# Kernel tuning notes

Measured on AMD Instinct MI355X. Metric: run time of the kernel, lower is better.

Reference implementation:

```python
import jax, jax.numpy as jnp
import numpy as np
from jax import lax

B, N, C, H, W, D, BEV = 2, 6, 64, 128, 352, 48, 64


def _make_buffers():
    # depths: linspace(1,100,D) -> used with shape (1,1,D,1)
    depths = jnp.linspace(1.0, 100.0, D).reshape(1, 1, D, 1)
    y, x = jnp.meshgrid(jnp.arange(H), jnp.arange(W), indexing='ij')
    xy1 = jnp.stack((x.flatten(), y.flatten(), jnp.ones(H * W)), axis=0).astype(jnp.float32)  # (3, H*W)
    return depths, xy1


def setup_inputs() -> dict:
    key = jax.random.key(0)
    ks = jax.random.split(key, 8)
    image_features = jax.random.normal(ks[0], (B * N, C, H, W), jnp.float32)
    # realistic invertible pinhole intrinsics embedded in 4x4
    fx = 500.0 + 10.0 * jax.random.normal(ks[1], (B, N))
    fy = 500.0 + 10.0 * jax.random.normal(ks[2], (B, N))
    K = jnp.tile(jnp.eye(4, dtype=jnp.float32), (B, N, 1, 1))
    K = K.at[..., 0, 0].set(fx).at[..., 1, 1].set(fy)
    K = K.at[..., 0, 2].set(W / 2.0).at[..., 1, 2].set(H / 2.0)
    extrinsics = jnp.tile(jnp.eye(4, dtype=jnp.float32), (B, N, 1, 1)) + 0.01 * jax.random.normal(ks[3], (B, N, 4, 4))
    view_attention = jnp.ones((1, N, 1, H, W), jnp.float32)
    depth_attention = jnp.ones((1, D, 1, 1), jnp.float32)
    # kaiming-normal conv weights (fan_in mode, relu gain sqrt(2))
    c1w = jax.random.normal(ks[4], (BEV, 3, 3, 3), jnp.float32) * np.sqrt(2.0 / (3 * 9))
    c1b = jnp.zeros((BEV,), jnp.float32)
    c2w = jax.random.normal(ks[5], (BEV, BEV, 3, 3), jnp.float32) * np.sqrt(2.0 / (BEV * 9))
    c2b = jnp.zeros((BEV,), jnp.float32)
    bn1_g = jnp.ones((BEV,), jnp.float32); bn1_b = jnp.zeros((BEV,), jnp.float32)
    bn2_g = jnp.ones((BEV,), jnp.float32); bn2_b = jnp.zeros((BEV,), jnp.float32)
    depths, xy1 = _make_buffers()
    return dict(image_features=image_features, intrinsics=K, extrinsics=extrinsics,
                view_attention=view_attention, depth_attention=depth_attention,
                c1w=c1w, c1b=c1b, bn1_g=bn1_g, bn1_b=bn1_b,
                c2w=c2w, c2b=c2b, bn2_g=bn2_g, bn2_b=bn2_b,
                depths=depths, xy1=xy1)


def _conv3x3(x, w, b):
    y = lax.conv_general_dilated(x, w, (1, 1), 'SAME',
                                 dimension_numbers=('NCHW', 'OIHW', 'NCHW'))
    return y + b.reshape(1, -1, 1, 1)


def _bn_train(x, g, b, eps=1e-5):
    # torch BatchNorm2d in training mode: biased batch stats over (B,H,W)
    m = x.mean(axis=(0, 2, 3), keepdims=True)
    v = x.var(axis=(0, 2, 3), keepdims=True)
    return g.reshape(1, -1, 1, 1) * (x - m) * lax.rsqrt(v + eps) + b.reshape(1, -1, 1, 1)


def reference(image_features, intrinsics, extrinsics, view_attention, depth_attention,
              c1w, c1b, bn1_g, bn1_b, c2w, c2b, bn2_g, bn2_b, depths, xy1):
    BN = B * N
    # ---- lift ----
    K3 = intrinsics.reshape(BN, 4, 4)[:, :3, :3]
    Kinv = jnp.linalg.inv(K3)                          # (BN,3,3)
    rays = jnp.einsum('bij,jp->bip', Kinv, xy1)        # (BN,3,H*W)
    # depths (1,1,D,1) * rays (BN,3,1,HW) -> (BN,3,D,HW), then the original's
    # .view(B,N,3,H,W,D) (a raw row-major reshape, reproduced faithfully)
    pc = (depths * rays[:, :, None, :]).reshape(B, N, 3, H, W, D)
    # (depth_probs in the original is computed then discarded; omitted)
    # ---- splat (fused weighted reduction over N and D) ----
    da = jax.nn.softmax(depth_attention, axis=1).reshape(D)       # (D,)
    va = jax.nn.softmax(view_attention, axis=1)[0, :, 0]          # (N,H,W)
    bev_features = jnp.einsum('bnchwd,d,nhw->bchw', pc, da, va)   # (B,3,H,W)
    h = jax.nn.relu(_bn_train(_conv3x3(bev_features, c1w, c1b), bn1_g, bn1_b))
    bev = jax.nn.relu(_bn_train(_conv3x3(h, c2w, c2b), bn2_g, bn2_b))
    return pc, bev
```

## Files before the change

kernel.cpp:

```cpp
#include <hip/hip_runtime.h>

#define W_ 352
#define H_ 128
#define HW 45056
#define D_ 48
#define B_ 2
#define N_ 6
#define DHW (D_*HW)
#define PC_SIZE (36*DHW)
#define BHW (B_*HW)
#define BEVN (B_*64*HW)

#define WS_KINV 0
#define WS_SUM1 192
#define WS_SQ1  256
#define WS_SUM2 448
#define WS_SQ2  512

#define NPC_BLK (PC_SIZE/1024)
#define CH_H2B0 4096
#define CH_H2B1 (CH_H2B0 + BEVN/2048)

typedef unsigned short ushort_t;
typedef __attribute__((ext_vector_type(8))) short bf16x8;
typedef __attribute__((ext_vector_type(4))) float f32x4;
typedef __attribute__((ext_vector_type(8))) unsigned short u16x8;
typedef __attribute__((ext_vector_type(4))) unsigned short u16x4;

static __device__ inline ushort_t f2bf(float f) {
    union { float f; unsigned u; } v; v.f = f;
    unsigned r = v.u + 0x7FFF + ((v.u >> 16) & 1);
    return (ushort_t)(r >> 16);
}
static __device__ inline float bf2f(ushort_t u) {
    union { unsigned u; float f; } v; v.u = ((unsigned)u) << 16; return v.f;
}
static __device__ inline void invert3x3(const float* __restrict__ M, float* __restrict__ o) {
    float a = M[0], b = M[1], c = M[2];
    float d = M[4], e = M[5], f = M[6];
    float g = M[8], h = M[9], ii = M[10];
    float det = a*(e*ii - f*h) - b*(d*ii - f*g) + c*(d*h - e*g);
    float inv = 1.f / det;
    o[0] = (e*ii - f*h)*inv; o[1] = (c*h - b*ii)*inv; o[2] = (b*f - c*e)*inv;
    o[3] = (f*g - d*ii)*inv; o[4] = (a*ii - c*g)*inv; o[5] = (c*d - a*f)*inv;
    o[6] = (d*h - e*g)*inv;  o[7] = (b*g - a*h)*inv;  o[8] = (a*e - b*d)*inv;
}

static __device__ inline void pc_write(int pcblk, const float* __restrict__ ws,
                                       const float* __restrict__ depths,
                                       float* __restrict__ out) {
    int f = pcblk * 1024 + (int)threadIdx.x * 4;
    int bnc = f / DHW;
    int r1  = f - bnc * DHW;
    int d   = r1 / HW;
    int p   = r1 - d * HW;
    int y   = p / W_;
    int x   = p - y * W_;
    float ka = ws[WS_KINV + bnc * 3 + 0];
    float kb = ws[WS_KINV + bnc * 3 + 1];
    float kc = ws[WS_KINV + bnc * 3 + 2];
    float dep = depths[d];
    float base = fmaf(kb, (float)y, kc);
    f32x4 v;
    v.x = dep * fmaf(ka, (float)(x + 0), base);
    v.y = dep * fmaf(ka, (float)(x + 1), base);
    v.z = dep * fmaf(ka, (float)(x + 2), base);
    v.w = dep * fmaf(ka, (float)(x + 3), base);
    __builtin_nontemporal_store(v, (f32x4*)(out + f));
}

__global__ __launch_bounds__(256) void k_fused1(const float* __restrict__ K4,
                                                const float* __restrict__ datt,
                                                const float* __restrict__ vatt,
                                                const float* __restrict__ depths,
                                                const float* __restrict__ w1,
                                                const float* __restrict__ b1,
                                                const float* __restrict__ w2,
                                                float* __restrict__ ws,
                                                ushort_t* __restrict__ h1pm,
                                                ushort_t* __restrict__ packedW) {
    int bid = blockIdx.x, tid = threadIdx.x;
    if (bid >= 352) {
        int e = (bid - 352) * 256 + tid;
        int tap = e >> 12;
        int r   = e & 4095;
        int n   = r >> 6, k = r & 63;
        int slot = (k >> 3) ^ (n & 7);
        packedW[tap * 4096 + n * 64 + slot * 8 + (k & 7)] = f2bf(w2[(n * 64 + k) * 9 + tap]);
        return;
    }
    if (bid == 0 && tid >= 128 && tid < 140)
        invert3x3(K4 + (tid - 128) * 16, ws + WS_KINV + (tid - 128) * 9);

    __shared__ float sBev[3][10][34];
    __shared__ float wl[64 * 27];
    __shared__ float sDep[48], sDa[48], sKinv[54];
    __shared__ __align__(16) ushort_t sTile[256 * 64];
    __shared__ float sSum[64], sSq[64];

    int b  = bid / 176;
    int t0 = bid - b * 176;
    int ty = t0 / 11, tx = t0 - ty * 11;
    int y0 = ty * 8, x0 = tx * 32;

    if (tid < 48) sDep[tid] = depths[tid];
    if (tid < 64) { sSum[tid] = 0.f; sSq[tid] = 0.f; }
    if (tid >= 64 && tid < 70) invert3x3(K4 + (b * 6 + tid - 64) * 16, sKinv + (tid - 64) * 9);
    if (tid == 192) {
        float mx = -1e30f;
        for (int k = 0; k < D_; k++) mx = fmaxf(mx, datt[k]);
        float s = 0.f, e[D_];
        for (int k = 0; k < D_; k++) { e[k] = expf(datt[k] - mx); s += e[k]; }
        float invs = 1.f / s;
        for (int k = 0; k < D_; k++) sDa[k] = e[k] * invs;
    }
    for (int i = tid; i < 64 * 27; i += 256) wl[i] = w1[i];
    __syncthreads();

    for (int idx = tid; idx < 340; idx += 256) {
        int hy = idx / 34, hx = idx - hy * 34;
        int py = y0 + hy - 1, px = x0 + hx - 1;
        float a0 = 0.f, a1 = 0.f, a2 = 0.f;
        if ((unsigned)py < H_ && (unsigned)px < W_) {
            int pix = py * W_ + px;
            float va[N_]; float mx = -1e30f;
            for (int n = 0; n < N_; n++) { va[n] = vatt[n * HW + pix]; mx = fmaxf(mx, va[n]); }
            float s = 0.f;
            for (int n = 0; n < N_; n++) { va[n] = expf(va[n] - mx); s += va[n]; }
            float invs = 1.f / s;
            int q0 = pix * 48;
            int d = q0 / HW;
            int p = q0 - d * HW;
            int y = p / W_;
            int x = p - y * W_;
            float fx = (float)x, fy = (float)y;
            float S0 = 0.f, S1 = 0.f, S2 = 0.f;
            #pragma unroll
            for (int dd = 0; dd < D_; dd++) {
                float wq = sDa[dd] * sDep[d];
                S0 = fmaf(wq, fx, S0);
                S1 = fmaf(wq, fy, S1);
                S2 += wq;
                x++; fx += 1.f;
                if (x == W_) { x = 0; fx = 0.f; y++; fy += 1.f; if (y == H_) { y = 0; fy = 0.f; d++; } }
            }
            for (int n = 0; n < N_; n++) {
                float van = va[n] * invs;
                const float* kv = sKinv + n * 9;
                a0 = fmaf(van, fmaf(kv[0], S0, fmaf(kv[1], S1, kv[2] * S2)), a0);
                a1 = fmaf(van, fmaf(kv[3], S0, fmaf(kv[4], S1, kv[5] * S2)), a1);
                a2 = fmaf(van, fmaf(kv[6], S0, fmaf(kv[7], S1, kv[8] * S2)), a2);
            }
        }
        sBev[0][hy][hx] = a0;
        sBev[1][hy][hx] = a1;
        sBev[2][hy][hx] = a2;
    }
    __syncthreads();

    int oy = tid >> 5, ox = tid & 31;
    int y = y0 + oy, x = x0 + ox;
    float v[27];
    #pragma unroll
    for (int ci = 0; ci < 3; ci++)
        #pragma unroll
        for (int dy = 0; dy < 3; dy++)
            #pragma unroll
            for (int dx = 0; dx < 3; dx++)
                v[ci * 9 + dy * 3 + dx] = sBev[ci][oy + dy][ox + dx];
    u16x8 pack[8];
    #pragma unroll
    for (int co = 0; co < 64; co++) {
        float acc = b1[co];
        #pragma unroll
        for (int k = 0; k < 27; k++) acc = fmaf(wl[co * 27 + k], v[k], acc);
        pack[co >> 3][co & 7] = (short)f2bf(acc);
    }
    ushort_t* dst = h1pm + (size_t)(b * HW + y * W_ + x) * 64;
    #pragma unroll
    for (int j = 0; j < 8; j++) {
        *(u16x8*)(dst + j * 8) = pack[j];
        *(u16x8*)(&sTile[tid * 64 + j * 8]) = pack[j];
    }
    __syncthreads();

    int c8 = tid & 7;
    int lp = tid >> 3;
    float s[8] = {0,0,0,0,0,0,0,0}, q[8] = {0,0,0,0,0,0,0,0};
    for (int p = lp; p < 256; p += 32) {
        u16x8 vv = *(const u16x8*)(&sTile[p * 64 + c8 * 8]);
        #pragma unroll
        for (int e = 0; e < 8; e++) {
            float f = bf2f(vv[e]);
            s[e] += f;
            q[e] = fmaf(f, f, q[e]);
        }
    }
    #pragma unroll
    for (int e = 0; e < 8; e++) {
        s[e] += __shfl_xor(s[e], 8);  s[e] += __shfl_xor(s[e], 16); s[e] += __shfl_xor(s[e], 32);
        q[e] += __shfl_xor(q[e], 8);  q[e] += __shfl_xor(q[e], 16); q[e] += __shfl_xor(q[e], 32);
    }
    if ((tid & 56) == 0) {
        #pragma unroll
        for (int e = 0; e < 8; e++) {
            atomicAdd(&sSum[c8 * 8 + e], s[e]);
            atomicAdd(&sSq[c8 * 8 + e], q[e]);
        }
    }
    __syncthreads();
    if (tid < 64) {
        atomicAdd(ws + WS_SUM1 + tid, sSum[tid]);
        atomicAdd(ws + WS_SQ1 + tid, sSq[tid]);
    }
}

__global__ __launch_bounds__(256) void k_conv2(const ushort_t* __restrict__ h1pm,
                                               const ushort_t* __restrict__ packedW,
                                               const float* __restrict__ b2,
                                               const float* __restrict__ g1,
                                               const float* __restrict__ bb1,
                                               float* __restrict__ ws,
                                               ushort_t* __restrict__ h2b) {
    __shared__ __align__(16) ushort_t sA[204 * 64];
    __shared__ __align__(16) ushort_t sB[3 * 4096];
    __shared__ float sSc[64], sSh[64];
    __shared__ float sRs[4][64], sRq[4][64];

    const int tid = threadIdx.x;
    if (tid < 64) {
        const float invM = 1.f / (float)BHW;
        float m = ws[WS_SUM1 + tid] * invM;
        float var = ws[WS_SQ1 + tid] * invM - m * m;
        float sc = g1[tid] * rsqrtf(var + 1e-5f);
        sSc[tid] = sc;
        sSh[tid] = bb1[tid] - m * sc;
    }
    __syncthreads();

    const int bid = blockIdx.x;
    const int b  = bid / 352;
    const int r0 = bid - b * 352;
    const int yb = r0 / 11;
    const int xb = r0 - yb * 11;
    const int x0 = xb * 32;
    const int y0 = yb * 4;
    const ushort_t* h1p = h1pm + (size_t)b * HW * 64;

    for (int idx = tid; idx < 204 * 8; idx += 256) {
        int r  = idx >> 3;
        int c8 = idx & 7;
        int hy = r / 34;
        int hx = r - hy * 34;
        int py = y0 + hy - 1, px = x0 + hx - 1;
        u16x8 ov = {0, 0, 0, 0, 0, 0, 0, 0};
        if ((unsigned)py < H_ && (unsigned)px < W_) {
            u16x8 v = *(const u16x8*)(h1p + (size_t)(py * W_ + px) * 64 + c8 * 8);
            #pragma unroll
            for (int e = 0; e < 8; e++) {
                int ci = c8 * 8 + e;
                float f = fmaxf(fmaf(sSc[ci], bf2f(v[e]), sSh[ci]), 0.f);
                ov[e] = (short)f2bf(f);
            }
        }
        int slot = c8 ^ (r & 7);
        *(u16x8*)(&sA[r * 64 + slot * 8]) = ov;
    }

    const int w    = tid >> 6;
    const int lane = tid & 63;
    const int g    = lane >> 4;
    const int c16  = lane & 15;

    f32x4 acc[2][4];
    #pragma unroll
    for (int m = 0; m < 2; m++)
        #pragma unroll
        for (int n = 0; n < 4; n++)
            acc[m][n] = (f32x4){0.f, 0.f, 0.f, 0.f};

    for (int grp = 0; grp < 3; grp++) {
        __syncthreads();
        const uint4* src = (const uint4*)(packedW + grp * 3 * 4096);
        uint4* dst = (uint4*)sB;
        #pragma unroll
        for (int i = 0; i < 6; i++) dst[tid + 256 * i] = src[tid + 256 * i];
        __syncthreads();
        #pragma unroll
        for (int tt = 0; tt < 3; tt++) {
            bf16x8 afr[2][2];
            #pragma unroll
            for (int mrep = 0; mrep < 2; mrep++)
                #pragma unroll
                for (int kk = 0; kk < 2; kk++) {
                    int r = (w + grp) * 34 + tt + c16 + 16 * mrep;
                    int slot = (g + 4 * kk) ^ (r & 7);
                    afr[mrep][kk] = *(const bf16x8*)(&sA[r * 64 + slot * 8]);
                }
            #pragma unroll
            for (int nrep = 0; nrep < 4; nrep++) {
                int n = 16 * nrep + c16;
                #pragma unroll
                for (int kk = 0; kk < 2; kk++) {
                    int slot = (g + 4 * kk) ^ (n & 7);
                    bf16x8 bfr = *(const bf16x8*)(&sB[tt * 4096 + n * 64 + slot * 8]);
                    #pragma unroll
                    for (int mrep = 0; mrep < 2; mrep++)
                        acc[mrep][nrep] = __builtin_amdgcn_mfma_f32_16x16x32_bf16(
                            afr[mrep][kk], bfr, acc[mrep][nrep], 0, 0, 0);
                }
            }
        }
    }

    const int y = y0 + w;
    #pragma unroll
    for (int nrep = 0; nrep < 4; nrep++) {
        int co = 16 * nrep + c16;
        float bias = b2[co];
        ushort_t* dstrow = h2b + (size_t)(b * 64 + co) * HW + y * W_;
        float s = 0.f, q = 0.f;
        #pragma unroll
        for (int mrep = 0; mrep < 2; mrep++) {
            u16x4 ov;
            #pragma unroll
            for (int j = 0; j < 4; j++) {
                float val = acc[mrep][nrep][j] + bias;
                s += val;
                q = fmaf(val, val, q);
                ov[j] = f2bf(val);
            }
            *(u16x4*)(dstrow + x0 + 16 * mrep + g * 4) = ov;
        }
        s += __shfl_xor(s, 16); s += __shfl_xor(s, 32);
        q += __shfl_xor(q, 16); q += __shfl_xor(q, 32);
        if (g == 0) { sRs[w][co] = s; sRq[w][co] = q; }
    }
    __syncthreads();
    if (tid < 64) {
        float s = sRs[0][tid] + sRs[1][tid] + sRs[2][tid] + sRs[3][tid];
        float q = sRq[0][tid] + sRq[1][tid] + sRq[2][tid] + sRq[3][tid];
        atomicAdd(ws + WS_SUM2 + tid, s);
        atomicAdd(ws + WS_SQ2 + tid, q);
    }
}

__global__ __launch_bounds__(256) void k_tail(const float* __restrict__ depths,
                                              const float* __restrict__ ws,
                                              const float* __restrict__ g2,
                                              const float* __restrict__ bb2,
                                              float* __restrict__ out) {
    int bid = blockIdx.x, tid = threadIdx.x;
    if (bid >= CH_H2B0 && bid < CH_H2B1) {
        const ushort_t* h2b = (const ushort_t*)((const char*)out + ((size_t)CH_H2B0 * 4096));
        int f2 = (bid - CH_H2B0) * 2048 + tid * 8;
        int c = (f2 / HW) & 63;
        const float invM = 1.f / (float)BHW;
        float m = ws[WS_SUM2 + c] * invM;
        float var = ws[WS_SQ2 + c] * invM - m * m;
        float sc = g2[c] * rsqrtf(var + 1e-5f);
        float sh = bb2[c] - m * sc;
        u16x8 v = *(const u16x8*)(h2b + f2);
        float* bev = out + PC_SIZE;
        f32x4 a, d;
        a.x = fmaxf(fmaf(sc, bf2f(v[0]), sh), 0.f);
        a.y = fmaxf(fmaf(sc, bf2f(v[1]), sh), 0.f);
        a.z = fmaxf(fmaf(sc, bf2f(v[2]), sh), 0.f);
        a.w = fmaxf(fmaf(sc, bf2f(v[3]), sh), 0.f);
        d.x = fmaxf(fmaf(sc, bf2f(v[4]), sh), 0.f);
        d.y = fmaxf(fmaf(sc, bf2f(v[5]), sh), 0.f);
        d.z = fmaxf(fmaf(sc, bf2f(v[6]), sh), 0.f);
        d.w = fmaxf(fmaf(sc, bf2f(v[7]), sh), 0.f);
        *(f32x4*)(bev + f2) = a;
        *(f32x4*)(bev + f2 + 4) = d;
        __syncthreads();
        pc_write(bid, ws, depths, out);
        return;
    }
    pc_write(bid, ws, depths, out);
}

extern "C" void kernel_launch(void* const* d_in, const int* in_sizes, int n_in,
                              void* d_out, int out_size, void* d_ws, size_t ws_size,
                              hipStream_t stream) {
    const float* K4     = (const float*)d_in[1];
    const float* vatt   = (const float*)d_in[3];
    const float* datt   = (const float*)d_in[4];
    const float* c1w    = (const float*)d_in[5];
    const float* c1b    = (const float*)d_in[6];
    const float* g1     = (const float*)d_in[7];
    const float* bb1    = (const float*)d_in[8];
    const float* c2w    = (const float*)d_in[9];
    const float* c2b    = (const float*)d_in[10];
    const float* g2     = (const float*)d_in[11];
    const float* bb2    = (const float*)d_in[12];
    const float* depths = (const float*)d_in[13];

    float* ws  = (float*)d_ws;
    char* base = (char*)d_out;
    ushort_t* h1pm    = (ushort_t*)base;
    ushort_t* packedW = (ushort_t*)(base + (12u << 20));
    ushort_t* h2b     = (ushort_t*)(base + ((size_t)CH_H2B0 * 4096));

    hipMemsetAsync(ws, 0, 640 * sizeof(float), stream);
    k_fused1<<<496, 256, 0, stream>>>(K4, datt, vatt, depths, c1w, c1b, c2w, ws, h1pm, packedW);
    k_conv2 <<<704, 256, 0, stream>>>(h1pm, packedW, c2b, g1, bb1, ws, h2b);
    k_tail  <<<NPC_BLK, 256, 0, stream>>>(depths, ws, g2, bb2, (float*)d_out);
}
```

Before: 123.2 us.

## Closed-form depth sums, per-block BN partials, larger conv2 tiles, drop memset

```diff
diff --git a/kernel.cpp b/kernel.cpp
--- a/kernel.cpp
+++ b/kernel.cpp
@@ -12,14 +12,11 @@
 #define BEVN (B_*64*HW)
 
 #define WS_KINV 0
-#define WS_SUM1 192
-#define WS_SQ1  256
 #define WS_SUM2 448
 #define WS_SQ2  512
 
 #define NPC_BLK (PC_SIZE/1024)
 #define CH_H2B0 4096
-#define CH_H2B1 (CH_H2B0 + BEVN/2048)
 
 typedef unsigned short ushort_t;
 typedef __attribute__((ext_vector_type(8))) short bf16x8;
@@ -78,9 +75,11 @@
                                                 const float* __restrict__ w2,
                                                 float* __restrict__ ws,
                                                 ushort_t* __restrict__ h1pm,
-                                                ushort_t* __restrict__ packedW) {
+                                                ushort_t* __restrict__ packedW,
+                                                float* __restrict__ P1) {
     int bid = blockIdx.x, tid = threadIdx.x;
     if (bid >= 352) {
+        if (bid == 352 && tid < 128) ws[WS_SUM2 + tid] = 0.f;
         int e = (bid - 352) * 256 + tid;
         int tap = e >> 12;
         int r   = e & 4095;
@@ -95,6 +94,7 @@
     __shared__ float sBev[3][10][34];
     __shared__ float wl[64 * 27];
     __shared__ float sDep[48], sDa[48], sKinv[54];
+    __shared__ float sSumDa, sKsum;
     __shared__ __align__(16) ushort_t sTile[256 * 64];
     __shared__ float sSum[64], sSq[64];
 
@@ -112,7 +112,14 @@
         float s = 0.f, e[D_];
         for (int k = 0; k < D_; k++) { e[k] = expf(datt[k] - mx); s += e[k]; }
         float invs = 1.f / s;
-        for (int k = 0; k < D_; k++) sDa[k] = e[k] * invs;
+        float sum = 0.f, ks = 0.f;
+        for (int k = 0; k < D_; k++) {
+            float dv = e[k] * invs;
+            sDa[k] = dv;
+            sum += dv;
+            ks = fmaf(dv, (float)k, ks);
+        }
+        sSumDa = sum; sKsum = ks;
     }
     for (int i = tid; i < 64 * 27; i += 256) wl[i] = w1[i];
     __syncthreads();
@@ -133,16 +140,24 @@
             int p = q0 - d * HW;
             int y = p / W_;
             int x = p - y * W_;
-            float fx = (float)x, fy = (float)y;
-            float S0 = 0.f, S1 = 0.f, S2 = 0.f;
-            #pragma unroll
-            for (int dd = 0; dd < D_; dd++) {
-                float wq = sDa[dd] * sDep[d];
-                S0 = fmaf(wq, fx, S0);
-                S1 = fmaf(wq, fy, S1);
-                S2 += wq;
-                x++; fx += 1.f;
-                if (x == W_) { x = 0; fx = 0.f; y++; fy += 1.f; if (y == H_) { y = 0; fy = 0.f; d++; } }
+            float S0, S1, S2;
+            if (x <= W_ - 48) {
+                float dep = sDep[d];
+                S2 = dep * sSumDa;
+                S0 = dep * fmaf(sSumDa, (float)x, sKsum);
+                S1 = (float)y * S2;
+            } else {
+                float fx = (float)x, fy = (float)y;
+                S0 = 0.f; S1 = 0.f; S2 = 0.f;
+                #pragma unroll
+                for (int dd = 0; dd < D_; dd++) {
+                    float wq = sDa[dd] * sDep[d];
+                    S0 = fmaf(wq, fx, S0);
+                    S1 = fmaf(wq, fy, S1);
+                    S2 += wq;
+                    x++; fx += 1.f;
+                    if (x == W_) { x = 0; fx = 0.f; y++; fy += 1.f; if (y == H_) { y = 0; fy = 0.f; d++; } }
+                }
             }
             for (int n = 0; n < N_; n++) {
                 float van = va[n] * invs;
@@ -210,8 +225,8 @@
     }
     __syncthreads();
     if (tid < 64) {
-        atomicAdd(ws + WS_SUM1 + tid, sSum[tid]);
-        atomicAdd(ws + WS_SQ1 + tid, sSq[tid]);
+        P1[bid * 128 + tid]      = sSum[tid];
+        P1[bid * 128 + 64 + tid] = sSq[tid];
     }
 }
 
@@ -220,34 +235,48 @@
                                                const float* __restrict__ b2,
                                                const float* __restrict__ g1,
                                                const float* __restrict__ bb1,
+                                               const float* __restrict__ P1,
                                                float* __restrict__ ws,
                                                ushort_t* __restrict__ h2b) {
-    __shared__ __align__(16) ushort_t sA[204 * 64];
+    __shared__ __align__(16) ushort_t sA[340 * 64];
     __shared__ __align__(16) ushort_t sB[3 * 4096];
     __shared__ float sSc[64], sSh[64];
+    __shared__ float sPS[4][64], sPQ[4][64];
     __shared__ float sRs[4][64], sRq[4][64];
 
     const int tid = threadIdx.x;
+    {
+        int c = tid & 63, hf = tid >> 6;
+        float s = 0.f, q = 0.f;
+        #pragma unroll 4
+        for (int i = 0; i < 88; i++) {
+            const float* pp = P1 + (size_t)(hf * 88 + i) * 128;
+            s += pp[c];
+            q += pp[64 + c];
+        }
+        sPS[hf][c] = s; sPQ[hf][c] = q;
+    }
+    __syncthreads();
     if (tid < 64) {
         const float invM = 1.f / (float)BHW;
-        float m = ws[WS_SUM1 + tid] * invM;
-        float var = ws[WS_SQ1 + tid] * invM - m * m;
-        float sc = g1[tid] * rsqrtf(var + 1e-5f);
+        float m = (sPS[0][tid] + sPS[1][tid] + sPS[2][tid] + sPS[3][tid]) * invM;
+        float vv = (sPQ[0][tid] + sPQ[1][tid] + sPQ[2][tid] + sPQ[3][tid]) * invM - m * m;
+        float sc = g1[tid] * rsqrtf(vv + 1e-5f);
         sSc[tid] = sc;
         sSh[tid] = bb1[tid] - m * sc;
     }
     __syncthreads();
 
     const int bid = blockIdx.x;
-    const int b  = bid / 352;
-    const int r0 = bid - b * 352;
+    const int b  = bid / 176;
+    const int r0 = bid - b * 176;
     const int yb = r0 / 11;
     const int xb = r0 - yb * 11;
     const int x0 = xb * 32;
-    const int y0 = yb * 4;
+    const int y0 = yb * 8;
     const ushort_t* h1p = h1pm + (size_t)b * HW * 64;
 
-    for (int idx = tid; idx < 204 * 8; idx += 256) {
+    for (int idx = tid; idx < 340 * 8; idx += 256) {
         int r  = idx >> 3;
         int c8 = idx & 7;
         int hy = r / 34;
@@ -272,12 +301,14 @@
     const int g    = lane >> 4;
     const int c16  = lane & 15;
 
-    f32x4 acc[2][4];
-    #pragma unroll
-    for (int m = 0; m < 2; m++)
-        #pragma unroll
-        for (int n = 0; n < 4; n++)
-            acc[m][n] = (f32x4){0.f, 0.f, 0.f, 0.f};
+    f32x4 acc[2][2][4];
+    #pragma unroll
+    for (int l = 0; l < 2; l++)
+        #pragma unroll
+        for (int m = 0; m < 2; m++)
+            #pragma unroll
+            for (int n = 0; n < 4; n++)
+                acc[l][m][n] = (f32x4){0.f, 0.f, 0.f, 0.f};
 
     for (int grp = 0; grp < 3; grp++) {
         __syncthreads();
@@ -288,15 +319,17 @@
         __syncthreads();
         #pragma unroll
         for (int tt = 0; tt < 3; tt++) {
-            bf16x8 afr[2][2];
-            #pragma unroll
-            for (int mrep = 0; mrep < 2; mrep++)
+            bf16x8 afr[2][2][2];
+            #pragma unroll
+            for (int l = 0; l < 2; l++)
                 #pragma unroll
-                for (int kk = 0; kk < 2; kk++) {
-                    int r = (w + grp) * 34 + tt + c16 + 16 * mrep;
-                    int slot = (g + 4 * kk) ^ (r & 7);
-                    afr[mrep][kk] = *(const bf16x8*)(&sA[r * 64 + slot * 8]);
-                }
+                for (int mrep = 0; mrep < 2; mrep++)
+                    #pragma unroll
+                    for (int kk = 0; kk < 2; kk++) {
+                        int r = (w + 4 * l + grp) * 34 + tt + c16 + 16 * mrep;
+                        int slot = (g + 4 * kk) ^ (r & 7);
+                        afr[l][mrep][kk] = *(const bf16x8*)(&sA[r * 64 + slot * 8]);
+                    }
             #pragma unroll
             for (int nrep = 0; nrep < 4; nrep++) {
                 int n = 16 * nrep + c16;
@@ -305,32 +338,37 @@
                     int slot = (g + 4 * kk) ^ (n & 7);
                     bf16x8 bfr = *(const bf16x8*)(&sB[tt * 4096 + n * 64 + slot * 8]);
                     #pragma unroll
-                    for (int mrep = 0; mrep < 2; mrep++)
-                        acc[mrep][nrep] = __builtin_amdgcn_mfma_f32_16x16x32_bf16(
-                            afr[mrep][kk], bfr, acc[mrep][nrep], 0, 0, 0);
+                    for (int l = 0; l < 2; l++)
+                        #pragma unroll
+                        for (int mrep = 0; mrep < 2; mrep++)
+                            acc[l][mrep][nrep] = __builtin_amdgcn_mfma_f32_16x16x32_bf16(
+                                afr[l][mrep][kk], bfr, acc[l][mrep][nrep], 0, 0, 0);
                 }
             }
         }
     }
 
-    const int y = y0 + w;
     #pragma unroll
     for (int nrep = 0; nrep < 4; nrep++) {
         int co = 16 * nrep + c16;
         float bias = b2[co];
-        ushort_t* dstrow = h2b + (size_t)(b * 64 + co) * HW + y * W_;
         float s = 0.f, q = 0.f;
         #pragma unroll
-        for (int mrep = 0; mrep < 2; mrep++) {
-            u16x4 ov;
-            #pragma unroll
-            for (int j = 0; j < 4; j++) {
-                float val = acc[mrep][nrep][j] + bias;
-                s += val;
-                q = fmaf(val, val, q);
-                ov[j] = f2bf(val);
+        for (int l = 0; l < 2; l++) {
+            int y = y0 + w + 4 * l;
+            ushort_t* dstrow = h2b + (size_t)(b * 64 + co) * HW + y * W_;
+            #pragma unroll
+            for (int mrep = 0; mrep < 2; mrep++) {
+                u16x4 ov;
+                #pragma unroll
+                for (int j = 0; j < 4; j++) {
+                    float val = acc[l][mrep][nrep][j] + bias;
+                    s += val;
+                    q = fmaf(val, val, q);
+                    ov[j] = f2bf(val);
+                }
+                *(u16x4*)(dstrow + x0 + 16 * mrep + g * 4) = ov;
             }
-            *(u16x4*)(dstrow + x0 + 16 * mrep + g * 4) = ov;
         }
         s += __shfl_xor(s, 16); s += __shfl_xor(s, 32);
         q += __shfl_xor(q, 16); q += __shfl_xor(q, 32);
@@ -351,7 +389,7 @@
                                               const float* __restrict__ bb2,
                                               float* __restrict__ out) {
     int bid = blockIdx.x, tid = threadIdx.x;
-    if (bid >= CH_H2B0 && bid < CH_H2B1) {
+    if (bid >= CH_H2B0 && bid < CH_H2B0 + BEVN / 2048) {
         const ushort_t* h2b = (const ushort_t*)((const char*)out + ((size_t)CH_H2B0 * 4096));
         int f2 = (bid - CH_H2B0) * 2048 + tid * 8;
         int c = (f2 / HW) & 63;
@@ -400,10 +438,10 @@
     char* base = (char*)d_out;
     ushort_t* h1pm    = (ushort_t*)base;
     ushort_t* packedW = (ushort_t*)(base + (12u << 20));
+    float*    P1      = (float*)(base + (13u << 20));
     ushort_t* h2b     = (ushort_t*)(base + ((size_t)CH_H2B0 * 4096));
 
-    hipMemsetAsync(ws, 0, 640 * sizeof(float), stream);
-    k_fused1<<<496, 256, 0, stream>>>(K4, datt, vatt, depths, c1w, c1b, c2w, ws, h1pm, packedW);
-    k_conv2 <<<704, 256, 0, stream>>>(h1pm, packedW, c2b, g1, bb1, ws, h2b);
+    k_fused1<<<496, 256, 0, stream>>>(K4, datt, vatt, depths, c1w, c1b, c2w, ws, h1pm, packedW, P1);
+    k_conv2 <<<352, 256, 0, stream>>>(h1pm, packedW, c2b, g1, bb1, P1, ws, h2b);
     k_tail  <<<NPC_BLK, 256, 0, stream>>>(depths, ws, g2, bb2, (float*)d_out);
 }
```

Result: slower. 129.8 us (+5.3%).
